# Kernel optimization log

Hardware: AMD Instinct MI355X
Metric: run time of the kernel (lower is better)

The kernel has to match this reference:

```python
import jax, jax.numpy as jnp
import numpy as np

B, S, H = 2, 2048, 4096
NH, NKV, HD = 32, 8, 128
EPS = 1e-6


def _rope_tables(seq_len, head_dim, base=10000.0):
    inv = 1.0 / (base ** (np.arange(0, head_dim, 2, dtype=np.float32) / head_dim))
    t = np.arange(seq_len, dtype=np.float32)
    freqs = np.outer(t, inv)                       # [S, HD/2]
    emb = np.concatenate([freqs, freqs], axis=-1)  # [S, HD] (HF rotate_half layout)
    return jnp.asarray(np.cos(emb)), jnp.asarray(np.sin(emb))


def setup_inputs() -> dict:
    key = jax.random.key(0)
    ks = jax.random.split(key, 6)
    x = jax.random.normal(ks[0], (B, S, H), dtype=jnp.float32)
    wq = jax.random.normal(ks[1], (NH * HD, H), dtype=jnp.float32) * 0.02
    wk = jax.random.normal(ks[2], (NKV * HD, H), dtype=jnp.float32) * 0.02
    wv = jax.random.normal(ks[3], (NKV * HD, H), dtype=jnp.float32) * 0.02
    wo = jax.random.normal(ks[4], (H, NH * HD), dtype=jnp.float32) * 0.02
    cos1, sin1 = _rope_tables(S, HD)
    cos = jnp.broadcast_to(cos1[None], (B, S, HD))
    sin = jnp.broadcast_to(sin1[None], (B, S, HD))
    return {
        "x": x, "cos": cos, "sin": sin,
        "wq": wq, "wk": wk, "wv": wv, "wo": wo,
        "q_norm_w": jnp.ones((HD,), jnp.float32),
        "k_norm_w": jnp.ones((HD,), jnp.float32),
    }


def _rms_norm(x, w):
    # fp32 RMSNorm over last dim, scaled by per-head-dim weight
    xf = x.astype(jnp.float32)
    n = xf * jax.lax.rsqrt(jnp.mean(xf * xf, axis=-1, keepdims=True) + EPS)
    return n.astype(x.dtype) * w


def _rotate_half(x):
    x1, x2 = jnp.split(x, 2, axis=-1)
    return jnp.concatenate([-x2, x1], axis=-1)


def reference(x, cos, sin, wq, wk, wv, wo, q_norm_w, k_norm_w):
    bs, seqlen, _ = x.shape
    # projections (nn.Linear: y = x @ W^T)
    xq = (x @ wq.T).reshape(bs, seqlen, NH, HD)
    xk = (x @ wk.T).reshape(bs, seqlen, NKV, HD)
    xv = (x @ wv.T).reshape(bs, seqlen, NKV, HD)
    # per-head RMSNorm before RoPE
    xq = _rms_norm(xq, q_norm_w)
    xk = _rms_norm(xk, k_norm_w)
    # [b, h, s, d]
    xq = xq.transpose(0, 2, 1, 3)
    xk = xk.transpose(0, 2, 1, 3)
    xv = xv.transpose(0, 2, 1, 3)
    # RoPE, cos/sin broadcast over heads
    c = cos[:, None, :, :]
    s = sin[:, None, :, :]
    xq = xq * c + _rotate_half(xq) * s
    xk = xk * c + _rotate_half(xk) * s
    # GQA: repeat kv heads
    rep = NH // NKV
    if rep > 1:
        xk = jnp.repeat(xk, rep, axis=1)
        xv = jnp.repeat(xv, rep, axis=1)
    # causal SDPA
    scale = 1.0 / jnp.sqrt(jnp.float32(HD))
    scores = jnp.einsum("bhqd,bhkd->bhqk", xq, xk) * scale
    mask = jnp.tril(jnp.ones((seqlen, seqlen), bool))
    scores = jnp.where(mask, scores, jnp.finfo(scores.dtype).min)
    probs = jax.nn.softmax(scores, axis=-1)
    out = jnp.einsum("bhqk,bhkd->bhqd", probs, xv)
    out = out.transpose(0, 2, 1, 3).reshape(bs, seqlen, NH * HD)
    return out @ wo.T
```

## Files before the change

kernel.cpp:

```cpp
#include <hip/hip_runtime.h>
#include <hip/hip_bf16.h>

#define NB  2
#define SS  2048
#define HH  4096
#define NH  32
#define NKV 8
#define HD  128
#define MR  (NB*SS)

typedef __bf16 bf16x8 __attribute__((ext_vector_type(8)));
typedef float  f32x4  __attribute__((ext_vector_type(4)));
typedef float  f32x16 __attribute__((ext_vector_type(16)));
using bf16 = __hip_bfloat16;

__device__ __forceinline__ f32x4 mfma16(bf16x8 a, bf16x8 b, f32x4 c) {
  return __builtin_amdgcn_mfma_f32_16x16x32_bf16(a, b, c, 0, 0, 0);
}
__device__ __forceinline__ f32x16 mfma32(bf16x8 a, bf16x8 b, f32x16 c) {
  return __builtin_amdgcn_mfma_f32_32x32x16_bf16(a, b, c, 0, 0, 0);
}
__device__ __forceinline__ unsigned cvtpk(float lo, float hi) {
  unsigned r; asm("v_cvt_pk_bf16_f32 %0, %1, %2" : "=v"(r) : "v"(lo), "v"(hi));
  return r;
}
__device__ __forceinline__ void swap32(unsigned &a, unsigned &b) {
  asm volatile("v_permlane32_swap_b32 %0, %1" : "+v"(a), "+v"(b));
}
__device__ __forceinline__ float fexp2(float x) {
  float r; asm("v_exp_f32 %0, %1" : "=v"(r) : "v"(x)); return r;
}

typedef const __attribute__((address_space(1))) void gv_t;
typedef __attribute__((address_space(3))) void lv_t;
__device__ __forceinline__ void gload16(const void* g, void* l) {
  __builtin_amdgcn_global_load_lds((gv_t*)g, (lv_t*)l, 16, 0, 0);
}

__global__ void f2b(const float* __restrict__ s, bf16* __restrict__ d, int n)
{
  int i = blockIdx.x*blockDim.x + threadIdx.x;
  int stride = gridDim.x*blockDim.x;
  for (int idx = i*4; idx < n; idx += stride*4) {
    float4 v = *(const float4*)(s + idx);
    __hip_bfloat16 b0 = __float2bfloat16(v.x);
    __hip_bfloat16 b1 = __float2bfloat16(v.y);
    __hip_bfloat16 b2 = __float2bfloat16(v.z);
    __hip_bfloat16 b3 = __float2bfloat16(v.w);
    ushort4 o;
    o.x = *reinterpret_cast<unsigned short*>(&b0);
    o.y = *reinterpret_cast<unsigned short*>(&b1);
    o.z = *reinterpret_cast<unsigned short*>(&b2);
    o.w = *reinterpret_cast<unsigned short*>(&b3);
    *(ushort4*)((unsigned short*)d + idx) = o;
  }
}

template<typename OutT>
__global__ __launch_bounds__(512, 2) void gemm256(
    const bf16* __restrict__ A, const bf16* __restrict__ Bt, OutT* __restrict__ C,
    int M, int N, int K, int tilesX)
{
  __shared__ bf16 lds[2][2][2][256*32];

  const int bid = blockIdx.x;
  const int cpx = gridDim.x >> 3;
  const int wg  = (bid & 7)*cpx + (bid >> 3);
  const int m0 = (wg / tilesX) * 256, n0 = (wg % tilesX) * 256;

  const int tid = threadIdx.x;
  const int l = tid & 63;
  const int l15 = l & 15, lhi = l >> 4;
  const int wid = tid >> 6;
  const int wr = wid >> 2, wc = wid & 3;

  const int srow  = tid >> 2;
  const int sslot = tid & 3;
  const int sxs   = sslot ^ (srow & 3);
  const bf16* ga0 = A  + (size_t)(m0 + srow)*K       + sxs*8;
  const bf16* ga1 = A  + (size_t)(m0 + srow + 128)*K + sxs*8;
  const bf16* gb0 = Bt + (size_t)(n0 + srow)*K       + sxs*8;
  const bf16* gb1 = Bt + (size_t)(n0 + srow + 128)*K + sxs*8;
  const int ldst = srow*32 + sslot*8;

#define STAGE(buf, s, kadd) do {                                  \
    gload16(ga0 + (kadd), &lds[buf][0][s][ldst]);                 \
    gload16(ga1 + (kadd), &lds[buf][0][s][ldst + 128*32]);        \
    gload16(gb0 + (kadd), &lds[buf][1][s][ldst]);                 \
    gload16(gb1 + (kadd), &lds[buf][1][s][ldst + 128*32]);        \
  } while (0)

  f32x4 acc[8][4];
  #pragma unroll
  for (int fm = 0; fm < 8; ++fm)
    #pragma unroll
    for (int fn = 0; fn < 4; ++fn)
      #pragma unroll
      for (int e = 0; e < 4; ++e) acc[fm][fn][e] = 0.f;

  const int slotoff = (lhi ^ (l15 & 3))*8;
  const int arow = wr*128 + l15;
  const int brow = wc*64  + l15;

  const int nt = K >> 6;
  STAGE(0, 0, 0);
  STAGE(0, 1, 32);
  asm volatile("s_waitcnt vmcnt(4)" ::: "memory");
  __builtin_amdgcn_s_barrier();

  for (int t = 0; t < nt; ++t) {
    const int p = t & 1;
    const bool pf = (t + 1 < nt);
    const int kn = (t + 1) << 6;
    #pragma unroll
    for (int s = 0; s < 2; ++s) {
      if (pf) {
        if (s == 0) STAGE(p ^ 1, 0, kn);
        else        STAGE(p ^ 1, 1, kn + 32);
      }
      bf16x8 af[8], bfr[4];
      #pragma unroll
      for (int fm = 0; fm < 8; ++fm)
        af[fm] = *(const bf16x8*)&lds[p][0][s][(arow + fm*16)*32 + slotoff];
      #pragma unroll
      for (int fn = 0; fn < 4; ++fn)
        bfr[fn] = *(const bf16x8*)&lds[p][1][s][(brow + fn*16)*32 + slotoff];
      __builtin_amdgcn_s_setprio(1);
      #pragma unroll
      for (int fm = 0; fm < 8; ++fm)
        #pragma unroll
        for (int fn = 0; fn < 4; ++fn)
          acc[fm][fn] = mfma16(af[fm], bfr[fn], acc[fm][fn]);
      __builtin_amdgcn_s_setprio(0);
      if (pf) asm volatile("s_waitcnt vmcnt(4)" ::: "memory");
      else    asm volatile("s_waitcnt vmcnt(0)" ::: "memory");
      __builtin_amdgcn_s_barrier();
    }
  }
#undef STAGE

  #pragma unroll
  for (int fm = 0; fm < 8; ++fm) {
    const int crow = m0 + wr*128 + fm*16 + lhi*4;
    #pragma unroll
    for (int fn = 0; fn < 4; ++fn) {
      const int ccol = n0 + wc*64 + fn*16 + l15;
      #pragma unroll
      for (int j = 0; j < 4; ++j) {
        if constexpr (sizeof(OutT) == 2)
          C[(size_t)(crow + j)*N + ccol] = __float2bfloat16(acc[fm][fn][j]);
        else
          C[(size_t)(crow + j)*N + ccol] = acc[fm][fn][j];
      }
    }
  }
}

__global__ __launch_bounds__(256) void normrope(
    const bf16* __restrict__ src, bf16* __restrict__ dst,
    const float* __restrict__ cosb, const float* __restrict__ sinb,
    const float* __restrict__ w, int nh, float scale, int rowstride, int coloff)
{
  const int wid = threadIdx.x >> 6, lane = threadIdx.x & 63;
  const int row = blockIdx.x*4 + wid;
  const int m = row / nh, h = row % nh;
  const int b = m / SS, s = m % SS;
  const bf16* sp = src + (size_t)m*rowstride + coloff + h*HD;
  float v1 = __bfloat162float(sp[lane]);
  float v2 = __bfloat162float(sp[lane + 64]);
  float ss = v1*v1 + v2*v2;
  #pragma unroll
  for (int msk = 1; msk < 64; msk <<= 1) ss += __shfl_xor(ss, msk);
  float r = rsqrtf(ss*(1.f/128.f) + 1e-6f) * scale;
  float n1 = v1*r*w[lane], n2 = v2*r*w[lane + 64];
  const float* cp  = cosb + (size_t)m*HD;
  const float* sip = sinb + (size_t)m*HD;
  float o1 = n1*cp[lane]      - n2*sip[lane];
  float o2 = n2*cp[lane + 64] + n1*sip[lane + 64];
  bf16* dp = dst + ((size_t)(b*nh + h)*SS + s)*HD;
  dp[lane]      = __float2bfloat16(o1);
  dp[lane + 64] = __float2bfloat16(o2);
}

__global__ __launch_bounds__(256) void vtrans(const bf16* __restrict__ v0,
                                              bf16* __restrict__ vt,
                                              int rowstride, int coloff)
{
  __shared__ bf16 tile[64][65];
  const int s0 = blockIdx.x*64, d0 = blockIdx.y*64, bkv = blockIdx.z;
  const int bb = bkv >> 3, kv = bkv & 7;
  const int c = threadIdx.x & 63, rbase = threadIdx.x >> 6;
  #pragma unroll
  for (int r = 0; r < 64; r += 4) {
    int sl = r + rbase;
    tile[sl][c] = v0[(size_t)(bb*SS + s0 + sl)*rowstride + coloff + kv*HD + d0 + c];
  }
  __syncthreads();
  #pragma unroll
  for (int r = 0; r < 64; r += 4) {
    int dl = r + rbase;
    vt[((size_t)bkv*HD + d0 + dl)*SS + s0 + c] = tile[c][dl];
  }
}

__global__ __launch_bounds__(512, 2) void attn_fwd(
    const bf16* __restrict__ qr, const bf16* __restrict__ kr,
    const bf16* __restrict__ vt, bf16* __restrict__ ao)
{
  __shared__ __align__(16) char smem[32768];
  char* KsB = smem;
  char* VsB = smem + 16384;

  const int L = blockIdx.x;
  const int orig = (L & 7)*64 + (L >> 3);
  const int bh = orig >> 3, j = orig & 7;
  const int b = bh >> 5, h = bh & 31, kvh = h >> 2;

  const int tid = threadIdx.x;
  const int wid = tid >> 6, lane = tid & 63;
  const int l31 = lane & 31, hi = lane >> 5;
  const unsigned hi16 = hi << 4;
  const unsigned swz = (lane & 7) << 4;

  const int qw0 = (wid < 4) ? (j*128 + wid*32) : ((15 - j)*128 + (wid - 4)*32);
  const int NT = 32 - 2*j;
  const int qlane = qw0 + l31;

  const bf16* Qp = qr + ((size_t)(b*NH + h)*SS + qlane)*HD;
  const bf16* Kp = kr + (size_t)(b*NKV + kvh)*SS*HD;
  const bf16* Vp = vt + (size_t)(b*NKV + kvh)*HD*SS;

  const int krow = tid >> 3;
  const int kslot = (tid & 7)*2;
  const int vrow = tid >> 2;
  const int vslot = (tid & 3)*2;
  const bf16* kg = Kp + (size_t)krow*HD + kslot*8;
  const bf16* vg = Vp + (size_t)vrow*SS + vslot*8;
  char* kl0 = KsB + krow*256 + (((unsigned)(kslot*16))     ^ ((krow & 7) << 4));
  char* kl1 = KsB + krow*256 + (((unsigned)((kslot+1)*16)) ^ ((krow & 7) << 4));
  char* vl0 = VsB + vrow*128 + (((unsigned)(vslot*16))     ^ ((vrow & 7) << 4));
  char* vl1 = VsB + vrow*128 + (((unsigned)((vslot+1)*16)) ^ ((vrow & 7) << 4));

  float4 kp0 = *(const float4*)(kg);
  float4 kp1 = *(const float4*)(kg + 8);
  float4 vp0 = *(const float4*)(vg);
  float4 vp1 = *(const float4*)(vg + 8);
  *(float4*)kl0 = kp0; *(float4*)kl1 = kp1;
  *(float4*)vl0 = vp0; *(float4*)vl1 = vp1;
  __syncthreads();

  bf16x8 qf[8];
  #pragma unroll
  for (int kd = 0; kd < 8; ++kd)
    qf[kd] = *(const bf16x8*)(Qp + kd*16 + hi*8);

  f32x16 o0, o1, o2, o3;
  #pragma unroll
  for (int r = 0; r < 16; ++r) { o0[r] = 0.f; o1[r] = 0.f; o2[r] = 0.f; o3[r] = 0.f; }
  float mrow = -1e30f, lrow = 0.f;

  for (int t = 0; t < NT; ++t) {
    const int kv0 = t*64;
    const bool haveNext = (t + 1 < NT);
    if (haveNext) {
      const bf16* kgn = kg + (size_t)(kv0 + 64)*HD;
      const bf16* vgn = vg + kv0 + 64;
      kp0 = *(const float4*)(kgn);
      kp1 = *(const float4*)(kgn + 8);
      vp0 = *(const float4*)(vgn);
      vp1 = *(const float4*)(vgn + 8);
    }

    if (kv0 <= qw0 + 31) {
      f32x16 s0, s1;
      #pragma unroll
      for (int r = 0; r < 16; ++r) { s0[r] = 0.f; s1[r] = 0.f; }
      #pragma unroll
      for (int kd = 0; kd < 8; ++kd) {
        bf16x8 k0f = *(const bf16x8*)(KsB + l31*256        + (((unsigned)(kd*32) + hi16) ^ swz));
        bf16x8 k1f = *(const bf16x8*)(KsB + (32 + l31)*256 + (((unsigned)(kd*32) + hi16) ^ swz));
        s0 = mfma32(k0f, qf[kd], s0);
        s1 = mfma32(k1f, qf[kd], s1);
      }
      if (kv0 + 63 > qw0) {
        #pragma unroll
        for (int r = 0; r < 16; ++r) {
          const int off = (r & 3) + 8*(r >> 2) + 4*hi;
          if (kv0 + off > qlane)      s0[r] = -1e30f;
          if (kv0 + 32 + off > qlane) s1[r] = -1e30f;
        }
      }
      float tmax = s0[0];
      #pragma unroll
      for (int r = 1; r < 16; ++r) tmax = fmaxf(tmax, s0[r]);
      #pragma unroll
      for (int r = 0; r < 16; ++r) tmax = fmaxf(tmax, s1[r]);
      tmax = fmaxf(tmax, __shfl_xor(tmax, 32));
      if (!__all(tmax <= mrow + 8.f)) {
        float mnew = fmaxf(mrow, tmax);
        float alpha = fexp2(mrow - mnew);
        mrow = mnew;
        lrow *= alpha;
        #pragma unroll
        for (int r = 0; r < 16; ++r) {
          o0[r] *= alpha; o1[r] *= alpha; o2[r] *= alpha; o3[r] *= alpha;
        }
      }
      float tsum = 0.f;
      #pragma unroll
      for (int r = 0; r < 16; ++r) { s0[r] = fexp2(s0[r] - mrow); tsum += s0[r]; }
      #pragma unroll
      for (int r = 0; r < 16; ++r) { s1[r] = fexp2(s1[r] - mrow); tsum += s1[r]; }
      tsum += __shfl_xor(tsum, 32);
      lrow += tsum;

      #pragma unroll
      for (int ks = 0; ks < 4; ++ks) {
        const int bb0 = (ks & 1)*8;
        float p0,p1,p2,p3,p4,p5,p6,p7;
        if (ks < 2) { p0=s0[bb0+0];p1=s0[bb0+1];p2=s0[bb0+2];p3=s0[bb0+3];
                      p4=s0[bb0+4];p5=s0[bb0+5];p6=s0[bb0+6];p7=s0[bb0+7]; }
        else        { p0=s1[bb0+0];p1=s1[bb0+1];p2=s1[bb0+2];p3=s1[bb0+3];
                      p4=s1[bb0+4];p5=s1[bb0+5];p6=s1[bb0+6];p7=s1[bb0+7]; }
        unsigned c01 = cvtpk(p0,p1), c23 = cvtpk(p2,p3);
        unsigned c45 = cvtpk(p4,p5), c67 = cvtpk(p6,p7);
        unsigned w0 = c01, w2 = c45; swap32(w0, w2);
        unsigned w1 = c23, w3 = c67; swap32(w1, w3);
        union { unsigned u[4]; bf16x8 v; } pa;
        pa.u[0]=w0; pa.u[1]=w1; pa.u[2]=w2; pa.u[3]=w3;
        #pragma unroll
        for (int dt = 0; dt < 4; ++dt) {
          bf16x8 vf = *(const bf16x8*)(VsB + (dt*32 + l31)*128 +
                                       (((unsigned)(ks*32) + hi16) ^ swz));
          f32x16 &oo = (dt==0)?o0:(dt==1)?o1:(dt==2)?o2:o3;
          oo = mfma32(vf, pa.v, oo);
        }
      }
    }

    __syncthreads();
    if (haveNext) {
      *(float4*)kl0 = kp0; *(float4*)kl1 = kp1;
      *(float4*)vl0 = vp0; *(float4*)vl1 = vp1;
    }
    __syncthreads();
  }

  const float invl = 1.f / lrow;
  char* ow = smem + wid*4096;
  bf16* aop = ao + ((size_t)b*SS + qlane)*HH + h*HD;
  const unsigned eswz = (l31 & 7) << 4;
  #pragma unroll
  for (int half = 0; half < 2; ++half) {
    #pragma unroll
    for (int hh = 0; hh < 2; ++hh) {
      #pragma unroll
      for (int r = 0; r < 16; ++r) {
        const int dcol = hh*32 + (r & 3) + 8*(r >> 2) + 4*hi;
        float val = ((half*2+hh)==0 ? o0[r] : (half*2+hh)==1 ? o1[r]
                     : (half*2+hh)==2 ? o2[r] : o3[r]) * invl;
        *(bf16*)(ow + l31*128 + (((unsigned)(dcol*2)) ^ eswz)) = __float2bfloat16(val);
      }
    }
    #pragma unroll
    for (int m = 0; m < 4; ++m) {
      const int c0 = hi*32 + m*8;
      bf16x8 vv = *(const bf16x8*)(ow + l31*128 + (((unsigned)(c0*2)) ^ eswz));
      *(bf16x8*)(aop + half*64 + c0) = vv;
    }
  }
}

extern "C" void kernel_launch(void* const* d_in, const int* in_sizes, int n_in,
                              void* d_out, int out_size, void* d_ws, size_t ws_size,
                              hipStream_t stream)
{
  const float* x    = (const float*)d_in[0];
  const float* cosb = (const float*)d_in[1];
  const float* sinb = (const float*)d_in[2];
  const float* wq   = (const float*)d_in[3];
  const float* wk   = (const float*)d_in[4];
  const float* wv   = (const float*)d_in[5];
  const float* wo   = (const float*)d_in[6];
  const float* qnw  = (const float*)d_in[7];
  const float* knw  = (const float*)d_in[8];
  float* out = (float*)d_out;

  char* ws = (char*)d_ws;
  bf16* xb  = (bf16*)(ws);
  bf16* wqb = (bf16*)(ws +  33554432);
  bf16* wkb = (bf16*)(ws +  67108864);
  bf16* wvb = (bf16*)(ws +  75497472);
  bf16* wob = (bf16*)(ws +  83886080);
  bf16* q0  = (bf16*)(ws + 117440512);
  bf16* kv0 = (bf16*)(ws + 150994944);
  bf16* qr  = (bf16*)(ws + 167772160);
  bf16* vt = xb;
  bf16* kr = wqb;
  bf16* ao = q0;

  f2b<<<2048, 256, 0, stream>>>(x,  xb,  MR*HH);
  f2b<<<2048, 256, 0, stream>>>(wq, wqb, NH*HD*HH);
  f2b<<<2048, 256, 0, stream>>>(wk, wkb, NKV*HD*HH);
  f2b<<<2048, 256, 0, stream>>>(wv, wvb, NKV*HD*HH);
  f2b<<<2048, 256, 0, stream>>>(wo, wob, HH*NH*HD);

  gemm256<bf16><<<256, 512, 0, stream>>>(xb, wqb, q0,  MR, 4096, HH, 16);
  gemm256<bf16><<<128, 512, 0, stream>>>(xb, wkb, kv0, MR, 2048, HH,  8);

  normrope<<<(MR*NH)/4,  256, 0, stream>>>(q0, qr, cosb, sinb, qnw, NH,
                                           0.08838834764831845f*1.44269504088896341f,
                                           4096, 0);
  normrope<<<(MR*NKV)/4, 256, 0, stream>>>(kv0, kr, cosb, sinb, knw, NKV, 1.0f,
                                           2048, 0);
  vtrans<<<dim3(32, 2, 16), 256, 0, stream>>>(kv0, vt, 2048, 1024);

  attn_fwd<<<512, 512, 0, stream>>>(qr, kr, vt, ao);

  gemm256<float><<<256, 512, 0, stream>>>(ao, wob, out, MR, HH, HH, 16);
}
```

Measured before the change: 588.2 us.

## Fuse QKV GEMMs, switch GEMM to 32x32 MFMA, async LDS loads in attention

Concatenates the Q, K and V weights so a single 384-block GEMM produces all three projections, replacing two launches that left the GPU underfilled. The GEMM moves from 16x16x32 to 32x32x16 MFMA tiles and splits each k-step into four quarter-stages with finer barriers. Attention now double-buffers K/V tiles through direct global-to-LDS loads instead of register staging. LDS use in attention doubles to 64KB, which may reduce occupancy, and the extra barriers add sync cost.

```diff
diff --git a/kernel.cpp b/kernel.cpp
--- a/kernel.cpp
+++ b/kernel.cpp
@@ -14,9 +14,6 @@
 typedef float  f32x16 __attribute__((ext_vector_type(16)));
 using bf16 = __hip_bfloat16;
 
-__device__ __forceinline__ f32x4 mfma16(bf16x8 a, bf16x8 b, f32x4 c) {
-  return __builtin_amdgcn_mfma_f32_16x16x32_bf16(a, b, c, 0, 0, 0);
-}
 __device__ __forceinline__ f32x16 mfma32(bf16x8 a, bf16x8 b, f32x16 c) {
   return __builtin_amdgcn_mfma_f32_32x32x16_bf16(a, b, c, 0, 0, 0);
 }
@@ -36,6 +33,7 @@
 __device__ __forceinline__ void gload16(const void* g, void* l) {
   __builtin_amdgcn_global_load_lds((gv_t*)g, (lv_t*)l, 16, 0, 0);
 }
+#define CFENCE asm volatile("" ::: "memory")
 
 __global__ void f2b(const float* __restrict__ s, bf16* __restrict__ d, int n)
 {
@@ -61,7 +59,7 @@
     const bf16* __restrict__ A, const bf16* __restrict__ Bt, OutT* __restrict__ C,
     int M, int N, int K, int tilesX)
 {
-  __shared__ bf16 lds[2][2][2][256*32];
+  __shared__ bf16 lds[2*2*2*8192];
 
   const int bid = blockIdx.x;
   const int cpx = gridDim.x >> 3;
@@ -70,7 +68,7 @@
 
   const int tid = threadIdx.x;
   const int l = tid & 63;
-  const int l15 = l & 15, lhi = l >> 4;
+  const int l31 = l & 31, hi = (l >> 5) & 1;
   const int wid = tid >> 6;
   const int wr = wid >> 2, wc = wid & 3;
 
@@ -83,74 +81,90 @@
   const bf16* gb1 = Bt + (size_t)(n0 + srow + 128)*K + sxs*8;
   const int ldst = srow*32 + sslot*8;
 
-#define STAGE(buf, s, kadd) do {                                  \
-    gload16(ga0 + (kadd), &lds[buf][0][s][ldst]);                 \
-    gload16(ga1 + (kadd), &lds[buf][0][s][ldst + 128*32]);        \
-    gload16(gb0 + (kadd), &lds[buf][1][s][ldst]);                 \
-    gload16(gb1 + (kadd), &lds[buf][1][s][ldst + 128*32]);        \
-  } while (0)
-
-  f32x4 acc[8][4];
-  #pragma unroll
-  for (int fm = 0; fm < 8; ++fm)
+#define REG(buf, ab, ks) (&lds[(((buf)*2 + (ab))*2 + (ks))*8192])
+#define STG_A(buf, ks, kofs) do { \
+    gload16(ga0 + (kofs), REG(buf,0,ks) + ldst); \
+    gload16(ga1 + (kofs), REG(buf,0,ks) + ldst + 128*32); } while(0)
+#define STG_B(buf, ks, kofs) do { \
+    gload16(gb0 + (kofs), REG(buf,1,ks) + ldst); \
+    gload16(gb1 + (kofs), REG(buf,1,ks) + ldst + 128*32); } while(0)
+
+  f32x16 acc[4][2];
+  #pragma unroll
+  for (int fm = 0; fm < 4; ++fm)
     #pragma unroll
-    for (int fn = 0; fn < 4; ++fn)
-      #pragma unroll
-      for (int e = 0; e < 4; ++e) acc[fm][fn][e] = 0.f;
-
-  const int slotoff = (lhi ^ (l15 & 3))*8;
-  const int arow = wr*128 + l15;
-  const int brow = wc*64  + l15;
+    for (int fn = 0; fn < 2; ++fn)
+      #pragma unroll
+      for (int e = 0; e < 16; ++e) acc[fm][fn][e] = 0.f;
+
+  const int arow = wr*128 + l31;
+  const int brow = wc*64  + l31;
+  const int sx3  = l31 & 3;
 
   const int nt = K >> 6;
-  STAGE(0, 0, 0);
-  STAGE(0, 1, 32);
+  STG_A(0, 0, 0); STG_B(0, 0, 0); STG_A(0, 1, 32); STG_B(0, 1, 32);
   asm volatile("s_waitcnt vmcnt(4)" ::: "memory");
   __builtin_amdgcn_s_barrier();
+  CFENCE;
 
   for (int t = 0; t < nt; ++t) {
-    const int p = t & 1;
-    const bool pf = (t + 1 < nt);
+    const int p = t & 1, nb = p ^ 1;
+    const bool pf = (t + 1) < nt;
     const int kn = (t + 1) << 6;
     #pragma unroll
-    for (int s = 0; s < 2; ++s) {
+    for (int q = 0; q < 4; ++q) {
       if (pf) {
-        if (s == 0) STAGE(p ^ 1, 0, kn);
-        else        STAGE(p ^ 1, 1, kn + 32);
-      }
-      bf16x8 af[8], bfr[4];
-      #pragma unroll
-      for (int fm = 0; fm < 8; ++fm)
-        af[fm] = *(const bf16x8*)&lds[p][0][s][(arow + fm*16)*32 + slotoff];
-      #pragma unroll
-      for (int fn = 0; fn < 4; ++fn)
-        bfr[fn] = *(const bf16x8*)&lds[p][1][s][(brow + fn*16)*32 + slotoff];
+        if      (q == 0) STG_A(nb, 0, kn);
+        else if (q == 1) STG_B(nb, 0, kn);
+        else if (q == 2) STG_A(nb, 1, kn + 32);
+        else             STG_B(nb, 1, kn + 32);
+      }
+      const int ks = q >> 1;
+      const int soff = (((q & 1)*2 + hi) ^ sx3)*8;
+      const bf16* Ar = REG(p, 0, ks);
+      const bf16* Br = REG(p, 1, ks);
+      bf16x8 af[4], bv[2];
+      #pragma unroll
+      for (int fm = 0; fm < 4; ++fm)
+        af[fm] = *(const bf16x8*)(Ar + (arow + fm*32)*32 + soff);
+      #pragma unroll
+      for (int fn = 0; fn < 2; ++fn)
+        bv[fn] = *(const bf16x8*)(Br + (brow + fn*32)*32 + soff);
+      __builtin_amdgcn_s_barrier();
+      CFENCE;
       __builtin_amdgcn_s_setprio(1);
       #pragma unroll
-      for (int fm = 0; fm < 8; ++fm)
+      for (int fm = 0; fm < 4; ++fm)
         #pragma unroll
-        for (int fn = 0; fn < 4; ++fn)
-          acc[fm][fn] = mfma16(af[fm], bfr[fn], acc[fm][fn]);
+        for (int fn = 0; fn < 2; ++fn)
+          acc[fm][fn] = mfma32(af[fm], bv[fn], acc[fm][fn]);
       __builtin_amdgcn_s_setprio(0);
-      if (pf) asm volatile("s_waitcnt vmcnt(4)" ::: "memory");
-      else    asm volatile("s_waitcnt vmcnt(0)" ::: "memory");
+      if (q == 1) {
+        if (pf) asm volatile("s_waitcnt vmcnt(4)" ::: "memory");
+        else    asm volatile("s_waitcnt vmcnt(0)" ::: "memory");
+      } else if (q == 3 && pf) {
+        asm volatile("s_waitcnt vmcnt(4)" ::: "memory");
+      }
       __builtin_amdgcn_s_barrier();
+      CFENCE;
     }
   }
-#undef STAGE
-
-  #pragma unroll
-  for (int fm = 0; fm < 8; ++fm) {
-    const int crow = m0 + wr*128 + fm*16 + lhi*4;
+#undef STG_A
+#undef STG_B
+#undef REG
+
+  #pragma unroll
+  for (int fm = 0; fm < 4; ++fm) {
     #pragma unroll
-    for (int fn = 0; fn < 4; ++fn) {
-      const int ccol = n0 + wc*64 + fn*16 + l15;
-      #pragma unroll
-      for (int j = 0; j < 4; ++j) {
+    for (int fn = 0; fn < 2; ++fn) {
+      const int ccol = n0 + wc*64 + fn*32 + l31;
+      #pragma unroll
+      for (int r = 0; r < 16; ++r) {
+        const int crow = m0 + wr*128 + fm*32 + (r & 3) + 8*(r >> 2) + 4*hi;
         if constexpr (sizeof(OutT) == 2)
-          C[(size_t)(crow + j)*N + ccol] = __float2bfloat16(acc[fm][fn][j]);
+          C[(size_t)crow*N + ccol] = __float2bfloat16(acc[fm][fn][r]);
         else
-          C[(size_t)(crow + j)*N + ccol] = acc[fm][fn][j];
+          C[(size_t)crow*N + ccol] = acc[fm][fn][r];
       }
     }
   }
@@ -207,9 +221,7 @@
     const bf16* __restrict__ qr, const bf16* __restrict__ kr,
     const bf16* __restrict__ vt, bf16* __restrict__ ao)
 {
-  __shared__ __align__(16) char smem[32768];
-  char* KsB = smem;
-  char* VsB = smem + 16384;
+  __shared__ __align__(16) char smem[65536];
 
   const int L = blockIdx.x;
   const int orig = (L & 7)*64 + (L >> 3);
@@ -230,29 +242,30 @@
   const bf16* Kp = kr + (size_t)(b*NKV + kvh)*SS*HD;
   const bf16* Vp = vt + (size_t)(b*NKV + kvh)*HD*SS;
 
-  const int krow = tid >> 3;
-  const int kslot = (tid & 7)*2;
-  const int vrow = tid >> 2;
-  const int vslot = (tid & 3)*2;
-  const bf16* kg = Kp + (size_t)krow*HD + kslot*8;
-  const bf16* vg = Vp + (size_t)vrow*SS + vslot*8;
-  char* kl0 = KsB + krow*256 + (((unsigned)(kslot*16))     ^ ((krow & 7) << 4));
-  char* kl1 = KsB + krow*256 + (((unsigned)((kslot+1)*16)) ^ ((krow & 7) << 4));
-  char* vl0 = VsB + vrow*128 + (((unsigned)(vslot*16))     ^ ((vrow & 7) << 4));
-  char* vl1 = VsB + vrow*128 + (((unsigned)((vslot+1)*16)) ^ ((vrow & 7) << 4));
-
-  float4 kp0 = *(const float4*)(kg);
-  float4 kp1 = *(const float4*)(kg + 8);
-  float4 vp0 = *(const float4*)(vg);
-  float4 vp1 = *(const float4*)(vg + 8);
-  *(float4*)kl0 = kp0; *(float4*)kl1 = kp1;
-  *(float4*)vl0 = vp0; *(float4*)vl1 = vp1;
-  __syncthreads();
-
+  const int krA = tid >> 4;
+  const int ksA = tid & 15;
+  const int vrA = tid >> 3;
+  const int vsA = tid & 7;
+  const int kswz = (ksA ^ (krA & 7))*8;
+  const int vswz = (vsA ^ (vrA & 7))*8;
+
+#define STAGE_ATTN(buf, kvbase) do {                                        \
+    char* kb = smem + (buf)*32768;                                          \
+    char* vb = kb + 16384;                                                  \
+    gload16(Kp + (size_t)(krA + (kvbase))*HD + kswz,      kb + tid*16);     \
+    gload16(Kp + (size_t)(krA + 32 + (kvbase))*HD + kswz, kb + 8192 + tid*16); \
+    gload16(Vp + (size_t)vrA*SS + (kvbase) + vswz,        vb + tid*16);     \
+    gload16(Vp + (size_t)(vrA + 64)*SS + (kvbase) + vswz, vb + 8192 + tid*16); \
+  } while (0)
+
+  STAGE_ATTN(0, 0);
   bf16x8 qf[8];
   #pragma unroll
   for (int kd = 0; kd < 8; ++kd)
     qf[kd] = *(const bf16x8*)(Qp + kd*16 + hi*8);
+  asm volatile("s_waitcnt vmcnt(0)" ::: "memory");
+  __builtin_amdgcn_s_barrier();
+  CFENCE;
 
   f32x16 o0, o1, o2, o3;
   #pragma unroll
@@ -260,16 +273,11 @@
   float mrow = -1e30f, lrow = 0.f;
 
   for (int t = 0; t < NT; ++t) {
+    const int p = t & 1;
+    const char* KsB = smem + p*32768;
+    const char* VsB = KsB + 16384;
+    if (t + 1 < NT) STAGE_ATTN(p ^ 1, (t + 1)*64);
     const int kv0 = t*64;
-    const bool haveNext = (t + 1 < NT);
-    if (haveNext) {
-      const bf16* kgn = kg + (size_t)(kv0 + 64)*HD;
-      const bf16* vgn = vg + kv0 + 64;
-      kp0 = *(const float4*)(kgn);
-      kp1 = *(const float4*)(kgn + 8);
-      vp0 = *(const float4*)(vgn);
-      vp1 = *(const float4*)(vgn + 8);
-    }
 
     if (kv0 <= qw0 + 31) {
       f32x16 s0, s1;
@@ -338,13 +346,11 @@
       }
     }
 
-    __syncthreads();
-    if (haveNext) {
-      *(float4*)kl0 = kp0; *(float4*)kl1 = kp1;
-      *(float4*)vl0 = vp0; *(float4*)vl1 = vp1;
-    }
-    __syncthreads();
-  }
+    asm volatile("s_waitcnt vmcnt(0)" ::: "memory");
+    __builtin_amdgcn_s_barrier();
+    CFENCE;
+  }
+#undef STAGE_ATTN
 
   const float invl = 1.f / lrow;
   char* ow = smem + wid*4096;
@@ -387,33 +393,29 @@
   float* out = (float*)d_out;
 
   char* ws = (char*)d_ws;
-  bf16* xb  = (bf16*)(ws);
-  bf16* wqb = (bf16*)(ws +  33554432);
-  bf16* wkb = (bf16*)(ws +  67108864);
-  bf16* wvb = (bf16*)(ws +  75497472);
-  bf16* wob = (bf16*)(ws +  83886080);
-  bf16* q0  = (bf16*)(ws + 117440512);
-  bf16* kv0 = (bf16*)(ws + 150994944);
-  bf16* qr  = (bf16*)(ws + 167772160);
+  bf16* xb    = (bf16*)(ws);
+  bf16* wqkvb = (bf16*)(ws +  33554432);
+  bf16* wob   = (bf16*)(ws +  83886080);
+  bf16* qkv0  = (bf16*)(ws + 117440512);
+  bf16* qr    = (bf16*)(ws + 167772160);
   bf16* vt = xb;
-  bf16* kr = wqb;
-  bf16* ao = q0;
+  bf16* kr = (bf16*)(ws + 8388608);
+  bf16* ao = qkv0;
 
   f2b<<<2048, 256, 0, stream>>>(x,  xb,  MR*HH);
-  f2b<<<2048, 256, 0, stream>>>(wq, wqb, NH*HD*HH);
-  f2b<<<2048, 256, 0, stream>>>(wk, wkb, NKV*HD*HH);
-  f2b<<<2048, 256, 0, stream>>>(wv, wvb, NKV*HD*HH);
+  f2b<<<2048, 256, 0, stream>>>(wq, wqkvb,                      NH*HD*HH);
+  f2b<<<2048, 256, 0, stream>>>(wk, wqkvb + (size_t)4096*4096, NKV*HD*HH);
+  f2b<<<2048, 256, 0, stream>>>(wv, wqkvb + (size_t)5120*4096, NKV*HD*HH);
   f2b<<<2048, 256, 0, stream>>>(wo, wob, HH*NH*HD);
 
-  gemm256<bf16><<<256, 512, 0, stream>>>(xb, wqb, q0,  MR, 4096, HH, 16);
-  gemm256<bf16><<<128, 512, 0, stream>>>(xb, wkb, kv0, MR, 2048, HH,  8);
-
-  normrope<<<(MR*NH)/4,  256, 0, stream>>>(q0, qr, cosb, sinb, qnw, NH,
+  gemm256<bf16><<<384, 512, 0, stream>>>(xb, wqkvb, qkv0, MR, 6144, HH, 24);
+
+  normrope<<<(MR*NH)/4,  256, 0, stream>>>(qkv0, qr, cosb, sinb, qnw, NH,
                                            0.08838834764831845f*1.44269504088896341f,
-                                           4096, 0);
-  normrope<<<(MR*NKV)/4, 256, 0, stream>>>(kv0, kr, cosb, sinb, knw, NKV, 1.0f,
-                                           2048, 0);
-  vtrans<<<dim3(32, 2, 16), 256, 0, stream>>>(kv0, vt, 2048, 1024);
+                                           6144, 0);
+  normrope<<<(MR*NKV)/4, 256, 0, stream>>>(qkv0, kr, cosb, sinb, knw, NKV, 1.0f,
+                                           6144, 4096);
+  vtrans<<<dim3(32, 2, 16), 256, 0, stream>>>(qkv0, vt, 6144, 5120);
 
   attn_fwd<<<512, 512, 0, stream>>>(qr, kr, vt, ao);
 
```

Measured after the change: 671.7 us. +14.2%, slower.
